# Kernel tuning notes

Hardware: AMD Instinct MI355X
Metric: run time of the kernel (lower is better)

## Reference

```python
import jax, jax.numpy as jnp
import numpy as np

DIM = 256
HEADS = 8
DIM_HEAD = 64
INNER = HEADS * DIM_HEAD  # 512
B, N = 4, 1024


def setup_inputs() -> dict:
    key = jax.random.key(0)
    ks = jax.random.split(key, 7)
    x = jax.random.normal(ks[0], (B, N, DIM), dtype=jnp.float32)
    attn_bias = jax.random.normal(ks[1], (B, HEADS, N, N), dtype=jnp.float32)
    s = 1.0 / np.sqrt(DIM)
    Wq = jax.random.normal(ks[2], (DIM, INNER), dtype=jnp.float32) * s
    Wkv = jax.random.normal(ks[3], (DIM, 2 * INNER), dtype=jnp.float32) * s
    # to_out initialized to zero in the torch module; use small random so output is non-trivial
    Wo = jax.random.normal(ks[4], (INNER, DIM), dtype=jnp.float32) * (1.0 / np.sqrt(INNER))
    bo = jnp.zeros((DIM,), dtype=jnp.float32)
    # gating initialized weight=0, bias=1 -> sigmoid(1); use small random weight + bias 1
    Wg = jax.random.normal(ks[5], (DIM, INNER), dtype=jnp.float32) * 0.02
    bg = jnp.ones((INNER,), dtype=jnp.float32)
    return {"x": x, "attn_bias": attn_bias, "Wq": Wq, "Wkv": Wkv,
            "Wo": Wo, "bo": bo, "Wg": Wg, "bg": bg}


def reference(x, attn_bias, Wq, Wkv, Wo, bo, Wg, bg):
    b, n, _ = x.shape
    scale = DIM_HEAD ** -0.5
    q = x @ Wq                                    # [b, n, inner]
    kv = x @ Wkv                                  # [b, n, 2*inner]
    k, v = jnp.split(kv, 2, axis=-1)
    def split_heads(t):
        return t.reshape(b, n, HEADS, DIM_HEAD).transpose(0, 2, 1, 3)  # [b,h,n,d]
    q, k, v = split_heads(q) * scale, split_heads(k), split_heads(v)
    dots = jnp.einsum('bhid,bhjd->bhij', q, k) + attn_bias
    # explicit max-subtract then softmax (matches original; numerically identical)
    attn = jax.nn.softmax(dots, axis=-1)
    out = jnp.einsum('bhij,bhjd->bhid', attn, v)  # [b,h,n,d]
    out = out.transpose(0, 2, 1, 3).reshape(b, n, INNER)
    gates = jax.nn.sigmoid(x @ Wg + bg)
    out = out * gates
    return out @ Wo + bo
```

## Files before the change

### kernel.cpp

```cpp
#include <hip/hip_runtime.h>

typedef unsigned short u16;
typedef unsigned int u32;
typedef __attribute__((ext_vector_type(8))) __bf16 bf16x8;
typedef __attribute__((ext_vector_type(4))) float floatx4;

#define DEV __device__ __forceinline__

DEV u16 f2bf(float f) {
  u32 u = __builtin_bit_cast(u32, f);
  u = (u + 0x7fffu + ((u >> 16) & 1u)) >> 16;
  return (u16)u;
}
DEV float bf2f(u16 h) {
  u32 u = ((u32)h) << 16;
  return __builtin_bit_cast(float, u);
}
DEV floatx4 MFMA(bf16x8 a, bf16x8 b, floatx4 c) {
  return __builtin_amdgcn_mfma_f32_16x16x32_bf16(a, b, c, 0, 0, 0);
}

__global__ void convert_k(const float* __restrict__ x, const float* __restrict__ Wq,
                          const float* __restrict__ Wkv, const float* __restrict__ Wg,
                          const float* __restrict__ Wo,
                          u16* __restrict__ xb, u16* __restrict__ WcatT, u16* __restrict__ WoT) {
  int i = blockIdx.x * 256 + threadIdx.x;
  if (i < 1048576) { xb[i] = f2bf(x[i]); return; }
  i -= 1048576;
  if (i < 524288) {
    int n = i >> 8, kk = i & 255;
    float v;
    if (n < 512) v = Wq[kk * 512 + n];
    else if (n < 1536) v = Wkv[kk * 1024 + (n - 512)];
    else v = Wg[kk * 512 + (n - 1536)];
    WcatT[i] = f2bf(v);
    return;
  }
  i -= 524288;
  if (i < 131072) {
    int n = i >> 9, kk = i & 511;
    WoT[i] = f2bf(Wo[kk * 256 + n]);
  }
}

__global__ __launch_bounds__(256) void gemm_qkvg(
    const u16* __restrict__ xb, const u16* __restrict__ WcatT, const float* __restrict__ bg,
    u16* __restrict__ qb, u16* __restrict__ kb, u16* __restrict__ vb, u16* __restrict__ gb) {
  __shared__ __attribute__((aligned(16))) u16 As[128 * 40];
  __shared__ __attribute__((aligned(16))) u16 Bs[128 * 40];
  const int tid = threadIdx.x;
  const int wave = tid >> 6, lane = tid & 63;
  const int lane15 = lane & 15, quad = lane >> 4;
  const int rm0 = blockIdx.x * 128;
  const int cn0 = blockIdx.y * 128;
  const int wm = (wave & 1) * 64, wn = (wave >> 1) * 64;
  const int arow = tid >> 2;
  const int aseg = (tid & 3) * 8;
  floatx4 acc[4][4] = {};
#pragma unroll 1
  for (int k0 = 0; k0 < 256; k0 += 32) {
#pragma unroll
    for (int p = 0; p < 2; ++p) {
      int row = arow + p * 64;
      uint4 va = *(const uint4*)(xb + (rm0 + row) * 256 + k0 + aseg);
      *(uint4*)(As + row * 40 + aseg) = va;
      uint4 vbv = *(const uint4*)(WcatT + (cn0 + row) * 256 + k0 + aseg);
      *(uint4*)(Bs + row * 40 + aseg) = vbv;
    }
    __syncthreads();
    bf16x8 af[4], bfr[4];
#pragma unroll
    for (int mt = 0; mt < 4; ++mt) af[mt] = *(const bf16x8*)(As + (wm + mt * 16 + lane15) * 40 + quad * 8);
#pragma unroll
    for (int nt = 0; nt < 4; ++nt) bfr[nt] = *(const bf16x8*)(Bs + (wn + nt * 16 + lane15) * 40 + quad * 8);
#pragma unroll
    for (int mt = 0; mt < 4; ++mt)
#pragma unroll
      for (int nt = 0; nt < 4; ++nt)
        acc[mt][nt] = MFMA(af[mt], bfr[nt], acc[mt][nt]);
    __syncthreads();
  }
#pragma unroll
  for (int mt = 0; mt < 4; ++mt)
#pragma unroll
    for (int nt = 0; nt < 4; ++nt)
#pragma unroll
      for (int r = 0; r < 4; ++r) {
        int row = rm0 + wm + mt * 16 + quad * 4 + r;
        int col = cn0 + wn + nt * 16 + lane15;
        float v = acc[mt][nt][r];
        int b = row >> 10, n = row & 1023;
        if (col < 512) {
          int h = col >> 6, d = col & 63;
          qb[((b * 8 + h) * 1024 + n) * 64 + d] = f2bf(v * 0.125f);
        } else if (col < 1024) {
          int c = col - 512, h = c >> 6, d = c & 63;
          kb[((b * 8 + h) * 1024 + n) * 64 + d] = f2bf(v);
        } else if (col < 1536) {
          int c = col - 1024, h = c >> 6, d = c & 63;
          vb[((b * 8 + h) * 1024 + n) * 64 + d] = f2bf(v);
        } else {
          int c = col - 1536;
          float g = 1.0f / (1.0f + __expf(-(v + bg[c])));
          gb[row * 512 + c] = f2bf(g);
        }
      }
}

__global__ __launch_bounds__(256) void vtrans_k(const u16* __restrict__ vb, u16* __restrict__ vT) {
  __shared__ __attribute__((aligned(16))) u16 L[64 * 72];
  const int bh = blockIdx.x, n0 = blockIdx.y * 64;
  const int t = threadIdx.x;
  const int row = t >> 2, seg = t & 3;
  const uint4* src = (const uint4*)(vb + ((size_t)bh * 1024 + n0 + row) * 64 + seg * 16);
  *(uint4*)(L + row * 72 + seg * 16) = src[0];
  *(uint4*)(L + row * 72 + seg * 16 + 8) = src[1];
  __syncthreads();
  const int d = t >> 2, jb = (t & 3) * 16;
  u16 tmp[16];
#pragma unroll
  for (int e = 0; e < 16; ++e) tmp[e] = L[(jb + e) * 72 + d];
  uint4* dst = (uint4*)(vT + ((size_t)bh * 64 + d) * 1024 + n0 + jb);
  dst[0] = *(uint4*)(tmp);
  dst[1] = *(uint4*)(tmp + 8);
}

__global__ __launch_bounds__(256, 2) void attn_k(
    const u16* __restrict__ qb, const u16* __restrict__ kb, const u16* __restrict__ vT,
    const float* __restrict__ bias, const u16* __restrict__ gb, u16* __restrict__ outgb) {
  __shared__ __attribute__((aligned(16))) u16 Ps[4 * 16 * 136];
  const int tid = threadIdx.x;
  const int wave = tid >> 6, lane = tid & 63;
  const int lane15 = lane & 15, quad = lane >> 4;
  const int bh = blockIdx.x;
  const int q0 = blockIdx.y * 64;

  bf16x8 qf0, qf1;
  {
    const u16* qrow = qb + ((size_t)(bh * 1024 + q0 + wave * 16 + lane15)) * 64 + quad * 8;
    qf0 = *(const bf16x8*)(qrow);
    qf1 = *(const bf16x8*)(qrow + 32);
  }
  bf16x8 ones;
#pragma unroll
  for (int e = 0; e < 8; ++e) ones[e] = __builtin_bit_cast(__bf16, (u16)0x3F80);

  floatx4 oacc[4] = {};
  float m_run[4], l_run[4];
#pragma unroll
  for (int r = 0; r < 4; ++r) { m_run[r] = -1e38f; l_run[r] = 0.f; }

  u16* Pw = Ps + wave * (16 * 136);
  const u16* kp = kb + (size_t)bh * 65536;
  const u16* vp = vT + (size_t)bh * 65536;
  const float* bb = bias + ((size_t)(bh * 1024 + q0 + wave * 16 + quad * 4)) * 1024;

#pragma unroll 1
  for (int kt = 0; kt < 8; ++kt) {
    const int kb0 = kt * 128;
    bf16x8 kf0[8], kf1[8];
#pragma unroll
    for (int nt = 0; nt < 8; ++nt) {
      const u16* kr = kp + ((size_t)(kb0 + nt * 16 + lane15)) * 64 + quad * 8;
      kf0[nt] = *(const bf16x8*)kr;
      kf1[nt] = *(const bf16x8*)(kr + 32);
    }
    float bv[8][4];
#pragma unroll
    for (int nt = 0; nt < 8; ++nt)
#pragma unroll
      for (int r = 0; r < 4; ++r)
        bv[nt][r] = bb[(size_t)r * 1024 + kb0 + nt * 16 + lane15];
    bf16x8 vf[4][4];
#pragma unroll
    for (int dt = 0; dt < 4; ++dt)
#pragma unroll
      for (int ck = 0; ck < 4; ++ck)
        vf[dt][ck] = *(const bf16x8*)(vp + ((size_t)(dt * 16 + lane15)) * 1024 + kb0 + ck * 32 + quad * 8);

    floatx4 s[8];
#pragma unroll
    for (int nt = 0; nt < 8; ++nt) {
      floatx4 z = {};
      z = MFMA(qf0, kf0[nt], z);
      s[nt] = MFMA(qf1, kf1[nt], z);
#pragma unroll
      for (int r = 0; r < 4; ++r) s[nt][r] += bv[nt][r];
    }

    float alpha[4];
#pragma unroll
    for (int r = 0; r < 4; ++r) {
      float mx = s[0][r];
#pragma unroll
      for (int nt = 1; nt < 8; ++nt) mx = fmaxf(mx, s[nt][r]);
#pragma unroll
      for (int off = 1; off < 16; off <<= 1) mx = fmaxf(mx, __shfl_xor(mx, off, 64));
      float m_new = fmaxf(m_run[r], mx);
      alpha[r] = __expf(m_run[r] - m_new);
      m_run[r] = m_new;
#pragma unroll
      for (int nt = 0; nt < 8; ++nt) s[nt][r] = __expf(s[nt][r] - m_new);
    }
#pragma unroll
    for (int nt = 0; nt < 8; ++nt)
#pragma unroll
      for (int r = 0; r < 4; ++r)
        Pw[(quad * 4 + r) * 136 + nt * 16 + lane15] = f2bf(s[nt][r]);
    bf16x8 pf[4];
#pragma unroll
    for (int ck = 0; ck < 4; ++ck) pf[ck] = *(const bf16x8*)(Pw + lane15 * 136 + ck * 32 + quad * 8);

    floatx4 lacc = {};
#pragma unroll
    for (int ck = 0; ck < 4; ++ck) lacc = MFMA(pf[ck], ones, lacc);
#pragma unroll
    for (int r = 0; r < 4; ++r) {
      l_run[r] = l_run[r] * alpha[r] + lacc[r];
#pragma unroll
      for (int dt = 0; dt < 4; ++dt) oacc[dt][r] *= alpha[r];
    }
#pragma unroll
    for (int dt = 0; dt < 4; ++dt)
#pragma unroll
      for (int ck = 0; ck < 4; ++ck)
        oacc[dt] = MFMA(pf[ck], vf[dt][ck], oacc[dt]);
  }

  const int h = bh & 7, b = bh >> 3;
#pragma unroll
  for (int dt = 0; dt < 4; ++dt)
#pragma unroll
    for (int r = 0; r < 4; ++r) {
      int nrow = q0 + wave * 16 + quad * 4 + r;
      float v = oacc[dt][r] / l_run[r];
      int inner = h * 64 + dt * 16 + lane15;
      size_t idx = ((size_t)(b * 1024 + nrow)) * 512 + inner;
      float g = bf2f(gb[idx]);
      outgb[idx] = f2bf(v * g);
    }
}

__global__ __launch_bounds__(256) void gemm_out(
    const u16* __restrict__ og, const u16* __restrict__ WoT, const float* __restrict__ bo,
    float* __restrict__ out) {
  __shared__ __attribute__((aligned(16))) u16 As[128 * 40];
  __shared__ __attribute__((aligned(16))) u16 Bs[128 * 40];
  const int tid = threadIdx.x;
  const int wave = tid >> 6, lane = tid & 63;
  const int lane15 = lane & 15, quad = lane >> 4;
  const int rm0 = blockIdx.x * 128;
  const int cn0 = blockIdx.y * 128;
  const int wm = (wave & 1) * 64, wn = (wave >> 1) * 64;
  const int arow = tid >> 2;
  const int aseg = (tid & 3) * 8;
  floatx4 acc[4][4] = {};
#pragma unroll 1
  for (int k0 = 0; k0 < 512; k0 += 32) {
#pragma unroll
    for (int p = 0; p < 2; ++p) {
      int row = arow + p * 64;
      uint4 va = *(const uint4*)(og + (rm0 + row) * 512 + k0 + aseg);
      *(uint4*)(As + row * 40 + aseg) = va;
      uint4 vbv = *(const uint4*)(WoT + (cn0 + row) * 512 + k0 + aseg);
      *(uint4*)(Bs + row * 40 + aseg) = vbv;
    }
    __syncthreads();
    bf16x8 af[4], bfr[4];
#pragma unroll
    for (int mt = 0; mt < 4; ++mt) af[mt] = *(const bf16x8*)(As + (wm + mt * 16 + lane15) * 40 + quad * 8);
#pragma unroll
    for (int nt = 0; nt < 4; ++nt) bfr[nt] = *(const bf16x8*)(Bs + (wn + nt * 16 + lane15) * 40 + quad * 8);
#pragma unroll
    for (int mt = 0; mt < 4; ++mt)
#pragma unroll
      for (int nt = 0; nt < 4; ++nt)
        acc[mt][nt] = MFMA(af[mt], bfr[nt], acc[mt][nt]);
    __syncthreads();
  }
#pragma unroll
  for (int mt = 0; mt < 4; ++mt)
#pragma unroll
    for (int nt = 0; nt < 4; ++nt)
#pragma unroll
      for (int r = 0; r < 4; ++r) {
        int row = rm0 + wm + mt * 16 + quad * 4 + r;
        int col = cn0 + wn + nt * 16 + lane15;
        out[row * 256 + col] = acc[mt][nt][r] + bo[col];
      }
}

extern "C" void kernel_launch(void* const* d_in, const int* in_sizes, int n_in,
                              void* d_out, int out_size, void* d_ws, size_t ws_size,
                              hipStream_t stream) {
  const float* x = (const float*)d_in[0];
  const float* bias = (const float*)d_in[1];
  const float* Wq = (const float*)d_in[2];
  const float* Wkv = (const float*)d_in[3];
  const float* Wo = (const float*)d_in[4];
  const float* bo = (const float*)d_in[5];
  const float* Wg = (const float*)d_in[6];
  const float* bg = (const float*)d_in[7];
  float* out = (float*)d_out;
  char* ws = (char*)d_ws;
  u16* xb    = (u16*)(ws);
  u16* WcatT = (u16*)(ws + 2097152);
  u16* WoT   = (u16*)(ws + 3145728);
  u16* qb    = (u16*)(ws + 3407872);
  u16* kb    = (u16*)(ws + 7602176);
  u16* vb    = (u16*)(ws + 11796480);
  u16* gb    = (u16*)(ws + 15990784);
  u16* ogb   = (u16*)(ws + 20185088);
  u16* vTb   = (u16*)(ws + 24379392);

  convert_k<<<6656, 256, 0, stream>>>(x, Wq, Wkv, Wg, Wo, xb, WcatT, WoT);
  dim3 g1(32, 16);
  gemm_qkvg<<<g1, 256, 0, stream>>>(xb, WcatT, bg, qb, kb, vb, gb);
  dim3 gv(32, 16);
  vtrans_k<<<gv, 256, 0, stream>>>(vb, vTb);
  dim3 g2(32, 16);
  attn_k<<<g2, 256, 0, stream>>>(qb, kb, vTb, bias, gb, ogb);
  dim3 g3(32, 2);
  gemm_out<<<g3, 256, 0, stream>>>(ogb, WoT, bo, out);
}
```

Baseline: 296.3 us.

## Split attention and output GEMM along K to raise parallelism, add merge kernels

```diff
diff --git a/kernel.cpp b/kernel.cpp
--- a/kernel.cpp
+++ b/kernel.cpp
@@ -43,47 +43,45 @@
   }
 }
 
-__global__ __launch_bounds__(256) void gemm_qkvg(
+__global__ __launch_bounds__(256, 4) void gemm_qkvg(
     const u16* __restrict__ xb, const u16* __restrict__ WcatT, const float* __restrict__ bg,
     u16* __restrict__ qb, u16* __restrict__ kb, u16* __restrict__ vb, u16* __restrict__ gb) {
   __shared__ __attribute__((aligned(16))) u16 As[128 * 40];
-  __shared__ __attribute__((aligned(16))) u16 Bs[128 * 40];
+  __shared__ __attribute__((aligned(16))) u16 Bs[64 * 40];
   const int tid = threadIdx.x;
   const int wave = tid >> 6, lane = tid & 63;
   const int lane15 = lane & 15, quad = lane >> 4;
   const int rm0 = blockIdx.x * 128;
-  const int cn0 = blockIdx.y * 128;
-  const int wm = (wave & 1) * 64, wn = (wave >> 1) * 64;
-  const int arow = tid >> 2;
-  const int aseg = (tid & 3) * 8;
-  floatx4 acc[4][4] = {};
+  const int cn0 = blockIdx.y * 64;
+  const int wm = (wave & 1) * 64, wn = (wave >> 1) * 32;
+  const int rowA = tid >> 1, segA = (tid & 1) * 16;
+  const int rowB = tid >> 2, segB = (tid & 3) * 8;
+  floatx4 acc[4][2] = {};
 #pragma unroll 1
   for (int k0 = 0; k0 < 256; k0 += 32) {
-#pragma unroll
-    for (int p = 0; p < 2; ++p) {
-      int row = arow + p * 64;
-      uint4 va = *(const uint4*)(xb + (rm0 + row) * 256 + k0 + aseg);
-      *(uint4*)(As + row * 40 + aseg) = va;
-      uint4 vbv = *(const uint4*)(WcatT + (cn0 + row) * 256 + k0 + aseg);
-      *(uint4*)(Bs + row * 40 + aseg) = vbv;
-    }
+    uint4 a0 = *(const uint4*)(xb + (rm0 + rowA) * 256 + k0 + segA);
+    uint4 a1 = *(const uint4*)(xb + (rm0 + rowA) * 256 + k0 + segA + 8);
+    uint4 b0 = *(const uint4*)(WcatT + (cn0 + rowB) * 256 + k0 + segB);
     __syncthreads();
-    bf16x8 af[4], bfr[4];
+    *(uint4*)(As + rowA * 40 + segA) = a0;
+    *(uint4*)(As + rowA * 40 + segA + 8) = a1;
+    *(uint4*)(Bs + rowB * 40 + segB) = b0;
+    __syncthreads();
+    bf16x8 af[4], bfr[2];
 #pragma unroll
     for (int mt = 0; mt < 4; ++mt) af[mt] = *(const bf16x8*)(As + (wm + mt * 16 + lane15) * 40 + quad * 8);
 #pragma unroll
-    for (int nt = 0; nt < 4; ++nt) bfr[nt] = *(const bf16x8*)(Bs + (wn + nt * 16 + lane15) * 40 + quad * 8);
+    for (int nt = 0; nt < 2; ++nt) bfr[nt] = *(const bf16x8*)(Bs + (wn + nt * 16 + lane15) * 40 + quad * 8);
 #pragma unroll
     for (int mt = 0; mt < 4; ++mt)
 #pragma unroll
-      for (int nt = 0; nt < 4; ++nt)
+      for (int nt = 0; nt < 2; ++nt)
         acc[mt][nt] = MFMA(af[mt], bfr[nt], acc[mt][nt]);
-    __syncthreads();
   }
 #pragma unroll
   for (int mt = 0; mt < 4; ++mt)
 #pragma unroll
-    for (int nt = 0; nt < 4; ++nt)
+    for (int nt = 0; nt < 2; ++nt)
 #pragma unroll
       for (int r = 0; r < 4; ++r) {
         int row = rm0 + wm + mt * 16 + quad * 4 + r;
@@ -125,15 +123,17 @@
   dst[1] = *(uint4*)(tmp + 8);
 }
 
-__global__ __launch_bounds__(256, 2) void attn_k(
+__global__ __launch_bounds__(256, 8) void attn_part_k(
     const u16* __restrict__ qb, const u16* __restrict__ kb, const u16* __restrict__ vT,
-    const float* __restrict__ bias, const u16* __restrict__ gb, u16* __restrict__ outgb) {
+    const float* __restrict__ bias,
+    float* __restrict__ po, float* __restrict__ pm, float* __restrict__ pl) {
   __shared__ __attribute__((aligned(16))) u16 Ps[4 * 16 * 136];
   const int tid = threadIdx.x;
   const int wave = tid >> 6, lane = tid & 63;
   const int lane15 = lane & 15, quad = lane >> 4;
   const int bh = blockIdx.x;
   const int q0 = blockIdx.y * 64;
+  const int kc = blockIdx.z;
 
   bf16x8 qf0, qf1;
   {
@@ -156,8 +156,8 @@
   const float* bb = bias + ((size_t)(bh * 1024 + q0 + wave * 16 + quad * 4)) * 1024;
 
 #pragma unroll 1
-  for (int kt = 0; kt < 8; ++kt) {
-    const int kb0 = kt * 128;
+  for (int kt = 0; kt < 2; ++kt) {
+    const int kb0 = kc * 256 + kt * 128;
     bf16x8 kf0[8], kf1[8];
 #pragma unroll
     for (int nt = 0; nt < 8; ++nt) {
@@ -227,67 +227,123 @@
         oacc[dt] = MFMA(pf[ck], vf[dt][ck], oacc[dt]);
   }
 
-  const int h = bh & 7, b = bh >> 3;
+  float* poW = po + ((size_t)(kc * 32 + bh)) * 65536;
 #pragma unroll
   for (int dt = 0; dt < 4; ++dt)
 #pragma unroll
     for (int r = 0; r < 4; ++r) {
-      int nrow = q0 + wave * 16 + quad * 4 + r;
-      float v = oacc[dt][r] / l_run[r];
-      int inner = h * 64 + dt * 16 + lane15;
-      size_t idx = ((size_t)(b * 1024 + nrow)) * 512 + inner;
-      float g = bf2f(gb[idx]);
-      outgb[idx] = f2bf(v * g);
-    }
-}
-
-__global__ __launch_bounds__(256) void gemm_out(
-    const u16* __restrict__ og, const u16* __restrict__ WoT, const float* __restrict__ bo,
-    float* __restrict__ out) {
+      int qrow = q0 + wave * 16 + quad * 4 + r;
+      poW[(size_t)qrow * 64 + dt * 16 + lane15] = oacc[dt][r];
+    }
+  if (lane15 == 0) {
+#pragma unroll
+    for (int r = 0; r < 4; ++r) {
+      int qrow = q0 + wave * 16 + quad * 4 + r;
+      pm[kc * 32768 + bh * 1024 + qrow] = m_run[r];
+      pl[kc * 32768 + bh * 1024 + qrow] = l_run[r];
+    }
+  }
+}
+
+__global__ __launch_bounds__(256) void attn_merge_k(
+    const float* __restrict__ po, const float* __restrict__ pm, const float* __restrict__ pl,
+    const u16* __restrict__ gb, u16* __restrict__ ogb) {
+  int t = blockIdx.x * 256 + threadIdx.x;
+  int row = t >> 4;
+  int dseg = (t & 15) * 4;
+  float m[4], l[4];
+#pragma unroll
+  for (int kc = 0; kc < 4; ++kc) {
+    m[kc] = pm[kc * 32768 + row];
+    l[kc] = pl[kc * 32768 + row];
+  }
+  float M = fmaxf(fmaxf(m[0], m[1]), fmaxf(m[2], m[3]));
+  float L = 0.f;
+  float w[4];
+#pragma unroll
+  for (int kc = 0; kc < 4; ++kc) { w[kc] = __expf(m[kc] - M); L += l[kc] * w[kc]; }
+  float4 O = {0.f, 0.f, 0.f, 0.f};
+#pragma unroll
+  for (int kc = 0; kc < 4; ++kc) {
+    float4 o = *(const float4*)(po + ((size_t)(kc * 32768 + row)) * 64 + dseg);
+    O.x += o.x * w[kc]; O.y += o.y * w[kc]; O.z += o.z * w[kc]; O.w += o.w * w[kc];
+  }
+  float inv = 1.0f / L;
+  int bh = row >> 10, q = row & 1023;
+  int h = bh & 7, b = bh >> 3;
+  size_t gi = ((size_t)(b * 1024 + q)) * 512 + h * 64 + dseg;
+  u16 g4[4];
+  *(uint2*)g4 = *(const uint2*)(gb + gi);
+  u16 r4[4];
+  r4[0] = f2bf(O.x * inv * bf2f(g4[0]));
+  r4[1] = f2bf(O.y * inv * bf2f(g4[1]));
+  r4[2] = f2bf(O.z * inv * bf2f(g4[2]));
+  r4[3] = f2bf(O.w * inv * bf2f(g4[3]));
+  *(uint2*)(ogb + gi) = *(uint2*)r4;
+}
+
+__global__ __launch_bounds__(256, 4) void gemm_out_part(
+    const u16* __restrict__ og, const u16* __restrict__ WoT, float* __restrict__ pout) {
   __shared__ __attribute__((aligned(16))) u16 As[128 * 40];
-  __shared__ __attribute__((aligned(16))) u16 Bs[128 * 40];
+  __shared__ __attribute__((aligned(16))) u16 Bs[64 * 40];
   const int tid = threadIdx.x;
   const int wave = tid >> 6, lane = tid & 63;
   const int lane15 = lane & 15, quad = lane >> 4;
   const int rm0 = blockIdx.x * 128;
-  const int cn0 = blockIdx.y * 128;
-  const int wm = (wave & 1) * 64, wn = (wave >> 1) * 64;
-  const int arow = tid >> 2;
-  const int aseg = (tid & 3) * 8;
-  floatx4 acc[4][4] = {};
+  const int cn0 = blockIdx.y * 64;
+  const int kc = blockIdx.z;
+  const int wm = (wave & 1) * 64, wn = (wave >> 1) * 32;
+  const int rowA = tid >> 1, segA = (tid & 1) * 16;
+  const int rowB = tid >> 2, segB = (tid & 3) * 8;
+  floatx4 acc[4][2] = {};
 #pragma unroll 1
-  for (int k0 = 0; k0 < 512; k0 += 32) {
-#pragma unroll
-    for (int p = 0; p < 2; ++p) {
-      int row = arow + p * 64;
-      uint4 va = *(const uint4*)(og + (rm0 + row) * 512 + k0 + aseg);
-      *(uint4*)(As + row * 40 + aseg) = va;
-      uint4 vbv = *(const uint4*)(WoT + (cn0 + row) * 512 + k0 + aseg);
-      *(uint4*)(Bs + row * 40 + aseg) = vbv;
-    }
+  for (int s = 0; s < 4; ++s) {
+    const int k0 = kc * 128 + s * 32;
+    uint4 a0 = *(const uint4*)(og + (rm0 + rowA) * 512 + k0 + segA);
+    uint4 a1 = *(const uint4*)(og + (rm0 + rowA) * 512 + k0 + segA + 8);
+    uint4 b0 = *(const uint4*)(WoT + (cn0 + rowB) * 512 + k0 + segB);
     __syncthreads();
-    bf16x8 af[4], bfr[4];
+    *(uint4*)(As + rowA * 40 + segA) = a0;
+    *(uint4*)(As + rowA * 40 + segA + 8) = a1;
+    *(uint4*)(Bs + rowB * 40 + segB) = b0;
+    __syncthreads();
+    bf16x8 af[4], bfr[2];
 #pragma unroll
     for (int mt = 0; mt < 4; ++mt) af[mt] = *(const bf16x8*)(As + (wm + mt * 16 + lane15) * 40 + quad * 8);
 #pragma unroll
-    for (int nt = 0; nt < 4; ++nt) bfr[nt] = *(const bf16x8*)(Bs + (wn + nt * 16 + lane15) * 40 + quad * 8);
+    for (int nt = 0; nt < 2; ++nt) bfr[nt] = *(const bf16x8*)(Bs + (wn + nt * 16 + lane15) * 40 + quad * 8);
 #pragma unroll
     for (int mt = 0; mt < 4; ++mt)
 #pragma unroll
-      for (int nt = 0; nt < 4; ++nt)
+      for (int nt = 0; nt < 2; ++nt)
         acc[mt][nt] = MFMA(af[mt], bfr[nt], acc[mt][nt]);
-    __syncthreads();
-  }
+  }
+  float* pw = pout + (size_t)kc * 1048576;
 #pragma unroll
   for (int mt = 0; mt < 4; ++mt)
 #pragma unroll
-    for (int nt = 0; nt < 4; ++nt)
+    for (int nt = 0; nt < 2; ++nt)
 #pragma unroll
       for (int r = 0; r < 4; ++r) {
         int row = rm0 + wm + mt * 16 + quad * 4 + r;
         int col = cn0 + wn + nt * 16 + lane15;
-        out[row * 256 + col] = acc[mt][nt][r] + bo[col];
+        pw[(size_t)row * 256 + col] = acc[mt][nt][r];
       }
+}
+
+__global__ __launch_bounds__(256) void reduce4_bo(
+    const float* __restrict__ pout, const float* __restrict__ bo, float* __restrict__ out) {
+  int g = blockIdx.x * 256 + threadIdx.x;
+  const float4* p = (const float4*)pout;
+  float4 s0 = p[g], s1 = p[g + 262144], s2 = p[g + 524288], s3 = p[g + 786432];
+  int col = (g * 4) & 255;
+  float4 bb = *(const float4*)(bo + col);
+  float4 r;
+  r.x = s0.x + s1.x + s2.x + s3.x + bb.x;
+  r.y = s0.y + s1.y + s2.y + s3.y + bb.y;
+  r.z = s0.z + s1.z + s2.z + s3.z + bb.z;
+  r.w = s0.w + s1.w + s2.w + s3.w + bb.w;
+  ((float4*)out)[g] = r;
 }
 
 extern "C" void kernel_launch(void* const* d_in, const int* in_sizes, int n_in,
@@ -312,14 +368,20 @@
   u16* gb    = (u16*)(ws + 15990784);
   u16* ogb   = (u16*)(ws + 20185088);
   u16* vTb   = (u16*)(ws + 24379392);
+  float* po  = (float*)(ws + 28573696);
+  float* pm  = (float*)(ws);
+  float* pl  = (float*)(ws + 524288);
+  float* pout = po;
 
   convert_k<<<6656, 256, 0, stream>>>(x, Wq, Wkv, Wg, Wo, xb, WcatT, WoT);
-  dim3 g1(32, 16);
+  dim3 g1(32, 32);
   gemm_qkvg<<<g1, 256, 0, stream>>>(xb, WcatT, bg, qb, kb, vb, gb);
   dim3 gv(32, 16);
   vtrans_k<<<gv, 256, 0, stream>>>(vb, vTb);
-  dim3 g2(32, 16);
-  attn_k<<<g2, 256, 0, stream>>>(qb, kb, vTb, bias, gb, ogb);
-  dim3 g3(32, 2);
-  gemm_out<<<g3, 256, 0, stream>>>(ogb, WoT, bo, out);
-}
+  dim3 g2(32, 16, 4);
+  attn_part_k<<<g2, 256, 0, stream>>>(qb, kb, vTb, bias, po, pm, pl);
+  attn_merge_k<<<2048, 256, 0, stream>>>(po, pm, pl, gb, ogb);
+  dim3 g3(32, 4, 4);
+  gemm_out_part<<<g3, 256, 0, stream>>>(ogb, WoT, pout);
+  reduce4_bo<<<1024, 256, 0, stream>>>(pout, bo, out);
+}
```

Result: slower. 347.1 us (+17.2%).
